# Optimization experiments

Hardware: AMD Instinct MI355X
Metric: run time of the kernel (lower is better)

Reference implementation:

```python
import jax, jax.numpy as jnp
import numpy as np

GX, GY, NH = 480, 360, 32
EPS = 1e-5


def _bn(x, g, b):
    # torch BatchNorm1d training-mode stats over the point dimension
    m = jnp.mean(x, axis=0)
    v = jnp.mean((x - m) ** 2, axis=0)
    return g * (x - m) / jnp.sqrt(v + EPS) + b


def setup_inputs():
    key = jax.random.key(0)
    ks = jax.random.split(key, 24)
    B, N, F = 2, 120000, 7
    s = 0.02
    inp = {
        "pt_fea": jax.random.normal(ks[0], (B, N, F), jnp.float32),
        "xy_ind": jax.random.randint(ks[1], (B, N, 2), 0, 360, dtype=jnp.int32),
        "bn0_g": jnp.ones((7,), jnp.float32), "bn0_b": jnp.zeros((7,), jnp.float32),
        "W1": jax.random.normal(ks[2], (7, 64), jnp.float32) * s,  "b1": jnp.zeros((64,), jnp.float32),
        "bn1_g": jnp.ones((64,), jnp.float32), "bn1_b": jnp.zeros((64,), jnp.float32),
        "W2": jax.random.normal(ks[3], (64, 128), jnp.float32) * s, "b2": jnp.zeros((128,), jnp.float32),
        "bn2_g": jnp.ones((128,), jnp.float32), "bn2_b": jnp.zeros((128,), jnp.float32),
        "W3": jax.random.normal(ks[4], (128, 256), jnp.float32) * s, "b3": jnp.zeros((256,), jnp.float32),
        "bn3_g": jnp.ones((256,), jnp.float32), "bn3_b": jnp.zeros((256,), jnp.float32),
        "W4": jax.random.normal(ks[5], (256, 512), jnp.float32) * s, "b4": jnp.zeros((512,), jnp.float32),
        "W5": jax.random.normal(ks[6], (512, NH), jnp.float32) * s, "b5": jnp.zeros((NH,), jnp.float32),
    }
    return inp


def _forward_sample(fea, xy, bn0_g, bn0_b, W1, b1, bn1_g, bn1_b, W2, b2,
                    bn2_g, bn2_b, W3, b3, bn3_g, bn3_b, W4, b4, W5, b5):
    # Simplified PointNet: BN -> (Linear, BN, ReLU) x3 -> Linear
    x = _bn(fea, bn0_g, bn0_b)
    x = jax.nn.relu(_bn(x @ W1 + b1, bn1_g, bn1_b))
    x = jax.nn.relu(_bn(x @ W2 + b2, bn2_g, bn2_b))
    x = jax.nn.relu(_bn(x @ W3 + b3, bn3_g, bn3_b))
    x = x @ W4 + b4                              # [N, 512]
    # per-voxel segment max over flattened BEV cell id
    ids = xy[:, 0] * GY + xy[:, 1]               # [N]
    nseg = GX * GY
    seg = jax.ops.segment_max(x, ids, num_segments=nseg)   # [nseg, 512]
    cnt = jax.ops.segment_sum(jnp.ones(ids.shape[0], x.dtype), ids, num_segments=nseg)
    occ = (cnt > 0)[:, None]
    seg = jnp.where(occ, seg, 0.0)               # empty voxels -> 0 (scatter semantics)
    nh = jax.nn.relu(seg @ W5 + b5)              # fea_compression
    nh = jnp.where(occ, nh, 0.0)
    return nh.reshape(GX, GY, NH).transpose(2, 0, 1)  # [NH, GX, GY]


def reference(pt_fea, xy_ind, bn0_g, bn0_b, W1, b1, bn1_g, bn1_b, W2, b2,
              bn2_g, bn2_b, W3, b3, bn3_g, bn3_b, W4, b4, W5, b5):
    f = lambda fea, xy: _forward_sample(fea, xy, bn0_g, bn0_b, W1, b1, bn1_g, bn1_b,
                                        W2, b2, bn2_g, bn2_b, W3, b3, bn3_g, bn3_b,
                                        W4, b4, W5, b5)
    return jax.vmap(f)(pt_fea, xy_ind)           # [B, NH, GX, GY]
```

## Files before the change

### kernel.cpp

```cpp
#include <hip/hip_runtime.h>
#include <cstdint>

#define GXD 480
#define GYD 360
#define NHD 32
#define NPTS 120000
#define MPAD 120064
#define MB128 (MPAD/128)
#define SEGR 129600
#define NSEG (GXD*GYD)
#define EPSB 1e-5f

using short8 = __attribute__((ext_vector_type(8))) short;
using f32x4  = __attribute__((ext_vector_type(4))) float;

__device__ __forceinline__ float bf2f(unsigned short u) {
    return __uint_as_float(((unsigned int)u) << 16);
}
__device__ __forceinline__ unsigned short f2bf(float f) {
    unsigned int u = __float_as_uint(f);
    u += 0x7fffu + ((u >> 16) & 1u);
    return (unsigned short)(u >> 16);
}
__device__ __forceinline__ unsigned int bnrelu_pack(unsigned int wv, float sc0, float sh0,
                                                    float sc1, float sh1)
{
    float lo = __uint_as_float(wv << 16);
    float hi = __uint_as_float(wv & 0xffff0000u);
    lo = fmaxf(fmaf(lo, sc0, sh0), 0.f);
    hi = fmaxf(fmaf(hi, sc1, sh1), 0.f);
    unsigned int r;
    asm("v_cvt_pk_bf16_f32 %0, %1, %2" : "=v"(r) : "v"(lo), "v"(hi));
    return r;
}

__device__ __forceinline__ void async16(const unsigned short* g, unsigned short* l)
{
    __builtin_amdgcn_global_load_lds(
        (const __attribute__((address_space(1))) unsigned int*)g,
        (__attribute__((address_space(3))) unsigned int*)l, 16, 0, 0);
}

__global__ __launch_bounds__(256) void bn0_stats_kernel(
    const float* __restrict__ fea, float* __restrict__ s0, float* __restrict__ q0)
{
    float s[7] = {0,0,0,0,0,0,0}, q[7] = {0,0,0,0,0,0,0};
    for (int p = blockIdx.x * 256 + threadIdx.x; p < NPTS; p += gridDim.x * 256) {
        const float* r = fea + (size_t)p * 7;
#pragma unroll
        for (int f = 0; f < 7; ++f) { float v = r[f]; s[f] += v; q[f] += v * v; }
    }
    __shared__ float red[256];
    int t = threadIdx.x;
#pragma unroll
    for (int f = 0; f < 7; ++f) {
        red[t] = s[f]; __syncthreads();
        for (int o = 128; o > 0; o >>= 1) {
            if (t < o) red[t] += red[t + o];
            __syncthreads();
        }
        if (t == 0) atomicAdd(&s0[f], red[0]);
        __syncthreads();
        red[t] = q[f]; __syncthreads();
        for (int o = 128; o > 0; o >>= 1) {
            if (t < o) red[t] += red[t + o];
            __syncthreads();
        }
        if (t == 0) atomicAdd(&q0[f], red[0]);
        __syncthreads();
    }
}

__global__ void prep0_kernel(const float* __restrict__ s0, const float* __restrict__ q0,
                             const float* __restrict__ g0, const float* __restrict__ b0,
                             const float* __restrict__ W1, const float* __restrict__ b1,
                             float* __restrict__ W1p, float* __restrict__ b1p)
{
    __shared__ float sc[7], sh[7];
    int t = threadIdx.x;
    if (t < 7) {
        float m = s0[t] / (float)NPTS;
        float v = q0[t] / (float)NPTS - m * m;
        float inv = 1.0f / sqrtf(fmaxf(v, 0.f) + EPSB);
        sc[t] = g0[t] * inv;
        sh[t] = b0[t] - m * g0[t] * inv;
    }
    __syncthreads();
    if (t < 64) {
        float acc = b1[t];
#pragma unroll
        for (int f = 0; f < 7; ++f) {
            W1p[f * 64 + t] = W1[f * 64 + t] * sc[f];
            acc += sh[f] * W1[f * 64 + t];
        }
        b1p[t] = acc;
    }
}

__global__ void prep_bn_kernel(const float* __restrict__ sum, const float* __restrict__ sq,
                               const float* __restrict__ g, const float* __restrict__ b,
                               float* __restrict__ sc, float* __restrict__ sh, int C)
{
    int c = blockIdx.x * blockDim.x + threadIdx.x;
    if (c < C) {
        float m = sum[c] / (float)NPTS;
        float v = sq[c] / (float)NPTS - m * m;
        float inv = 1.0f / sqrtf(fmaxf(v, 0.f) + EPSB);
        sc[c] = g[c] * inv;
        sh[c] = b[c] - m * g[c] * inv;
    }
}

template<int C>
__global__ __launch_bounds__(256) void bnrelu_kernel(
    unsigned short* __restrict__ Y,
    const float* __restrict__ sc, const float* __restrict__ sh)
{
    __shared__ float scs[C], shs[C];
    int t = threadIdx.x;
    for (int i = t; i < C; i += 256) { scs[i] = sc[i]; shs[i] = sh[i]; }
    __syncthreads();
    const size_t total8 = (size_t)MPAD * C / 8;
    for (size_t i = (size_t)blockIdx.x * 256 + t; i < total8; i += (size_t)gridDim.x * 256) {
        int c0 = (int)((i * 8) & (size_t)(C - 1));
        uint4 v = *(const uint4*)(Y + i * 8);
        float4 s0 = *(const float4*)&scs[c0];
        float4 s1 = *(const float4*)&scs[c0 + 4];
        float4 h0 = *(const float4*)&shs[c0];
        float4 h1 = *(const float4*)&shs[c0 + 4];
        uint4 o;
        o.x = bnrelu_pack(v.x, s0.x, h0.x, s0.y, h0.y);
        o.y = bnrelu_pack(v.y, s0.z, h0.z, s0.w, h0.w);
        o.z = bnrelu_pack(v.z, s1.x, h1.x, s1.y, h1.y);
        o.w = bnrelu_pack(v.w, s1.z, h1.z, s1.w, h1.w);
        *(uint4*)(Y + i * 8) = o;
    }
}

__global__ __launch_bounds__(256) void wtrans_kernel(const float* __restrict__ W,
                                                     unsigned short* __restrict__ Wt,
                                                     int K, int N)
{
    int i = blockIdx.x * 256 + threadIdx.x;
    if (i < K * N) {
        int k = i / N, n = i % N;
        Wt[(size_t)n * K + k] = f2bf(W[i]);
    }
}

__global__ __launch_bounds__(256) void layer1_kernel(
    const float* __restrict__ fea, const float* __restrict__ W1p, const float* __restrict__ b1p,
    unsigned short* __restrict__ y1, float* __restrict__ sum1, float* __restrict__ sq1)
{
    __shared__ float Wl[448], bl[64];
    __shared__ float feaL[256 * 7];
    __shared__ float colsum[64], colsq[64];
    int t = threadIdx.x;
    int p0 = blockIdx.x * 256;
    for (int i = t; i < 448; i += 256) Wl[i] = W1p[i];
    if (t < 64) { bl[t] = b1p[t]; colsum[t] = 0.f; colsq[t] = 0.f; }
    int nval7 = (NPTS - p0) * 7;
    for (int i = t; i < 256 * 7; i += 256)
        feaL[i] = (i < nval7) ? fea[(size_t)p0 * 7 + i] : 0.f;
    __syncthreads();
    int cg = t & 7, pt = t >> 3;
    float s[8] = {}, q[8] = {};
#pragma unroll
    for (int it = 0; it < 8; ++it) {
        int row = it * 32 + pt;
        bool valid = (p0 + row) < NPTS;
        float f[7];
#pragma unroll
        for (int ff = 0; ff < 7; ++ff) f[ff] = feaL[row * 7 + ff];
        float vj[8];
#pragma unroll
        for (int j = 0; j < 8; ++j) {
            int c = cg * 8 + j;
            float v = bl[c];
#pragma unroll
            for (int ff = 0; ff < 7; ++ff) v = fmaf(f[ff], Wl[ff * 64 + c], v);
            vj[j] = v;
            if (valid) { s[j] += v; q[j] += v * v; }
        }
        uint4 ow;
        ow.x = (unsigned int)f2bf(vj[0]) | ((unsigned int)f2bf(vj[1]) << 16);
        ow.y = (unsigned int)f2bf(vj[2]) | ((unsigned int)f2bf(vj[3]) << 16);
        ow.z = (unsigned int)f2bf(vj[4]) | ((unsigned int)f2bf(vj[5]) << 16);
        ow.w = (unsigned int)f2bf(vj[6]) | ((unsigned int)f2bf(vj[7]) << 16);
        *(uint4*)(y1 + (size_t)(p0 + row) * 64 + cg * 8) = ow;
    }
#pragma unroll
    for (int off = 8; off < 64; off <<= 1) {
#pragma unroll
        for (int j = 0; j < 8; ++j) {
            s[j] += __shfl_xor(s[j], off);
            q[j] += __shfl_xor(q[j], off);
        }
    }
    if ((t & 63) < 8) {
#pragma unroll
        for (int j = 0; j < 8; ++j) {
            atomicAdd(&colsum[cg * 8 + j], s[j]);
            atomicAdd(&colsq[cg * 8 + j], q[j]);
        }
    }
    __syncthreads();
    if (t < 64) {
        atomicAdd(&sum1[t], colsum[t]);
        atomicAdd(&sq1[t], colsq[t]);
    }
}

template<int K, int NC, bool STATS>
__global__ __launch_bounds__(256) void gemm_quad(
    const unsigned short* __restrict__ A, const unsigned short* __restrict__ Wt,
    const float* __restrict__ bias, unsigned short* __restrict__ Y,
    float* __restrict__ osum, float* __restrict__ osq)
{
    __shared__ __align__(16) unsigned short lds[16384];
    __shared__ float colsum[128], colsq[128];
    int t = threadIdx.x;
    int w = t >> 6, ln = t & 63, quad = ln >> 4, lr = ln & 15;
    int wr = w >> 1, wc = w & 1;
    const int mbase = blockIdx.y * 128;
    const int cbase = blockIdx.x * 128;
    unsigned short* Asl = lds;
    unsigned short* Bsl = lds + 8192;

    if (STATS && t < 128) { colsum[t] = 0.f; colsq[t] = 0.f; }
    __syncthreads();

    const int srow = w * 16 + (ln >> 2);
    const int koff = (ln & 3) * 8;

    auto stage = [&](int buf, int kt) {
#pragma unroll
        for (int half = 0; half < 2; ++half) {
            int row = half * 64 + srow;
            async16(A  + (size_t)(mbase + row) * K + kt + koff,
                    Asl + buf * 4096 + half * 2048 + w * 512 + ln * 8);
            async16(Wt + (size_t)(cbase + row) * K + kt + koff,
                    Bsl + buf * 4096 + half * 2048 + w * 512 + ln * 8);
        }
    };

    f32x4 acc[4][4];
#pragma unroll
    for (int i = 0; i < 4; ++i)
#pragma unroll
        for (int j = 0; j < 4; ++j) acc[i][j] = (f32x4){0.f, 0.f, 0.f, 0.f};

    stage(0, 0);
    stage(1, 32);

    constexpr int NR = K / 32;
#pragma unroll
    for (int r = 0; r < NR; ++r) {
        const int buf = r & 1;
        if (r + 1 < NR)
            asm volatile("s_waitcnt vmcnt(4)" ::: "memory");
        else
            asm volatile("s_waitcnt vmcnt(0)" ::: "memory");
        asm volatile("s_barrier" ::: "memory");
        short8 af[4], bfr[4];
#pragma unroll
        for (int mi = 0; mi < 4; ++mi)
            af[mi] = *(const short8*)&Asl[buf * 4096 + (wr * 64 + mi * 16 + lr) * 32 + quad * 8];
#pragma unroll
        for (int ni = 0; ni < 4; ++ni)
            bfr[ni] = *(const short8*)&Bsl[buf * 4096 + (wc * 64 + ni * 16 + lr) * 32 + quad * 8];
        asm volatile("s_waitcnt lgkmcnt(0)" ::: "memory");
        asm volatile("s_barrier" ::: "memory");
        if (r + 2 < NR)
            stage(buf, (r + 2) * 32);
#pragma unroll
        for (int mi = 0; mi < 4; ++mi)
#pragma unroll
            for (int ni = 0; ni < 4; ++ni)
                acc[mi][ni] = __builtin_amdgcn_mfma_f32_16x16x32_bf16(
                    af[mi], bfr[ni], acc[mi][ni], 0, 0, 0);
    }
    __syncthreads();

    unsigned short* Cw = lds + w * 4096;
#pragma unroll
    for (int ni = 0; ni < 4; ++ni) {
        int col = ni * 16 + lr;
        float bv = bias[cbase + wc * 64 + col];
        float s = 0.f, q = 0.f;
#pragma unroll
        for (int mi = 0; mi < 4; ++mi) {
            int rb = mi * 16 + quad * 4;
#pragma unroll
            for (int r = 0; r < 4; ++r) {
                float v = acc[mi][ni][r] + bv;
                Cw[(rb + r) * 64 + col] = f2bf(v);
                if (STATS && (mbase + wr * 64 + rb + r) < NPTS) { s += v; q += v * v; }
            }
        }
        if (STATS) {
            atomicAdd(&colsum[wc * 64 + col], s);
            atomicAdd(&colsq[wc * 64 + col], q);
        }
    }
#pragma unroll
    for (int i = 0; i < 8; ++i) {
        int idx = i * 64 + ln;
        int row = idx >> 3, colq = (idx & 7) * 8;
        *(uint4*)(Y + (size_t)(mbase + wr * 64 + row) * NC + cbase + wc * 64 + colq) =
            *(const uint4*)&Cw[row * 64 + colq];
    }
    if (STATS) {
        __syncthreads();
        if (t < 128) {
            atomicAdd(&osum[blockIdx.x * 128 + t], colsum[t]);
            atomicAdd(&osq[blockIdx.x * 128 + t], colsq[t]);
        }
    }
}

__global__ __launch_bounds__(256) void hist_kernel(const int* __restrict__ xy,
                                                   int* __restrict__ cnt)
{
    int p = blockIdx.x * 256 + threadIdx.x;
    if (p < NPTS) {
        int id = xy[(size_t)p * 2] * GYD + xy[(size_t)p * 2 + 1];
        atomicAdd(&cnt[id], 1);
    }
}

__global__ __launch_bounds__(256) void scanA_kernel(const int* __restrict__ cnt,
                                                    int* __restrict__ csum)
{
    __shared__ int red[256];
    int t = threadIdx.x, base = blockIdx.x * 2048;
    int s = 0;
    for (int i = t; i < 2048; i += 256) {
        int idx = base + i;
        if (idx < SEGR) s += cnt[idx];
    }
    red[t] = s; __syncthreads();
    for (int o = 128; o > 0; o >>= 1) { if (t < o) red[t] += red[t + o]; __syncthreads(); }
    if (t == 0) csum[blockIdx.x] = red[0];
}

__global__ void scanB_kernel(int* __restrict__ csum, int* __restrict__ offs)
{
    if (threadIdx.x == 0) {
        int run = 0;
        for (int i = 0; i < 64; ++i) { int v = csum[i]; csum[i] = run; run += v; }
        offs[SEGR] = run;
    }
}

__global__ __launch_bounds__(256) void scanC_kernel(const int* __restrict__ cnt,
                                                    const int* __restrict__ csum,
                                                    int* __restrict__ offs,
                                                    int* __restrict__ cursor)
{
    __shared__ int red[256];
    int t = threadIdx.x, base = blockIdx.x * 2048;
    int v[8]; int s = 0;
#pragma unroll
    for (int i = 0; i < 8; ++i) {
        int idx = base + t * 8 + i;
        v[i] = (idx < SEGR) ? cnt[idx] : 0;
        s += v[i];
    }
    red[t] = s; __syncthreads();
    for (int o = 1; o < 256; o <<= 1) {
        int x = (t >= o) ? red[t - o] : 0;
        __syncthreads();
        red[t] += x;
        __syncthreads();
    }
    int run = red[t] - s + csum[blockIdx.x];
#pragma unroll
    for (int i = 0; i < 8; ++i) {
        int idx = base + t * 8 + i;
        if (idx < SEGR) { offs[idx] = run; cursor[idx] = run; }
        run += v[i];
    }
}

__global__ __launch_bounds__(256) void scatter_idx_kernel(const int* __restrict__ xy,
                                                          int* __restrict__ cursor,
                                                          int* __restrict__ order)
{
    int p = blockIdx.x * 256 + threadIdx.x;
    if (p < NPTS) {
        int id = xy[(size_t)p * 2] * GYD + xy[(size_t)p * 2 + 1];
        int pos = atomicAdd(&cursor[id], 1);
        order[pos] = p;
    }
}

__global__ __launch_bounds__(256) void l4seg_kernel(
    const unsigned short* __restrict__ y3, const unsigned short* __restrict__ Wt4,
    const float* __restrict__ b4, const unsigned short* __restrict__ Wt5,
    const float* __restrict__ b5, const int* __restrict__ offs,
    const int* __restrict__ ord, float* __restrict__ out)
{
    __shared__ __align__(16) unsigned short Asl[2][2048];
    __shared__ __align__(16) unsigned short Bsl[2][4096];
    __shared__ __align__(16) unsigned short y4s[64 * 136];
    __shared__ __align__(16) unsigned short w5s[32 * 136];
    __shared__ float b4s[128];
    __shared__ int offs_s[65];
    int t = threadIdx.x;
    int w = t >> 6, ln = t & 63, quad = ln >> 4, lr = ln & 15;
    int c0 = blockIdx.x * 64;
    if (t < 65) offs_s[t] = offs[c0 + t];
    __syncthreads();
    const int jb = offs_s[0], je = offs_s[64];
    if (jb == je) {
#pragma unroll
        for (int j = 0; j < 8; ++j)
            out[(size_t)(w * 8 + j) * NSEG + c0 + ln] = 0.f;
        return;
    }
    const int cell = t >> 2, q = t & 3;
    const int cjb = offs_s[cell], cje = offs_s[cell + 1];

    f32x4 eacc[2];
    eacc[0] = (f32x4){0.f, 0.f, 0.f, 0.f};
    eacc[1] = (f32x4){0.f, 0.f, 0.f, 0.f};

    const int srow = w * 16 + (ln >> 2);
    const int koff = (ln & 3) * 8;

    for (int g = 0; g < 4; ++g) {
        {
            int n = t >> 3, ko = (t & 7) * 16;
            *(uint4*)&w5s[n * 136 + ko]     = *(const uint4*)(Wt5 + (size_t)n * 512 + g * 128 + ko);
            *(uint4*)&w5s[n * 136 + ko + 8] = *(const uint4*)(Wt5 + (size_t)n * 512 + g * 128 + ko + 8);
            if (t < 128) b4s[t] = b4[g * 128 + t];
        }
        float mxv[32];
#pragma unroll
        for (int i = 0; i < 32; ++i) mxv[i] = -3.0e38f;

        const unsigned short* Bg = Wt4 + (size_t)(g * 128 + srow) * 256 + koff;

        for (int cs = jb; cs < je; cs += 64) {
            int aj = cs + srow; if (aj >= je) aj = je - 1;
            const unsigned short* Ag = y3 + (size_t)ord[aj] * 256 + koff;
            auto stage = [&](int buf, int r) {
                async16(Ag + r * 32,            &Asl[buf][0] + w * 512 + ln * 8);
                async16(Bg + r * 32,            &Bsl[buf][0] + w * 512 + ln * 8);
                async16(Bg + 64 * 256 + r * 32, &Bsl[buf][2048] + w * 512 + ln * 8);
            };
            f32x4 acc[8];
#pragma unroll
            for (int i = 0; i < 8; ++i) acc[i] = (f32x4){0.f, 0.f, 0.f, 0.f};
            stage(0, 0); stage(1, 1);
#pragma unroll
            for (int r = 0; r < 8; ++r) {
                if (r < 7) asm volatile("s_waitcnt vmcnt(3)" ::: "memory");
                else       asm volatile("s_waitcnt vmcnt(0)" ::: "memory");
                asm volatile("s_barrier" ::: "memory");
                const int buf = r & 1;
                short8 af = *(const short8*)&Asl[buf][(w * 16 + lr) * 32 + quad * 8];
                short8 bfr[8];
#pragma unroll
                for (int ni = 0; ni < 8; ++ni)
                    bfr[ni] = *(const short8*)&Bsl[buf][(ni * 16 + lr) * 32 + quad * 8];
                asm volatile("s_waitcnt lgkmcnt(0)" ::: "memory");
                asm volatile("s_barrier" ::: "memory");
                if (r + 2 < 8) stage(buf, r + 2);
#pragma unroll
                for (int ni = 0; ni < 8; ++ni)
                    acc[ni] = __builtin_amdgcn_mfma_f32_16x16x32_bf16(af, bfr[ni], acc[ni], 0, 0, 0);
            }
#pragma unroll
            for (int ni = 0; ni < 8; ++ni) {
                float bv = b4s[ni * 16 + lr];
#pragma unroll
                for (int rr = 0; rr < 4; ++rr)
                    y4s[(w * 16 + quad * 4 + rr) * 136 + ni * 16 + lr] = f2bf(acc[ni][rr] + bv);
            }
            __syncthreads();
            int lo = cjb > cs ? cjb : cs;
            int hi = cje < cs + 64 ? cje : cs + 64;
            for (int j = lo; j < hi; ++j) {
                const uint4* rp = (const uint4*)&y4s[(j - cs) * 136 + q * 32];
#pragma unroll
                for (int u = 0; u < 4; ++u) {
                    uint4 vv = rp[u];
                    unsigned int wv[4] = {vv.x, vv.y, vv.z, vv.w};
#pragma unroll
                    for (int k2 = 0; k2 < 4; ++k2) {
                        int idx = u * 8 + k2 * 2;
                        mxv[idx]     = fmaxf(mxv[idx],     bf2f((unsigned short)(wv[k2] & 0xffffu)));
                        mxv[idx + 1] = fmaxf(mxv[idx + 1], bf2f((unsigned short)(wv[k2] >> 16)));
                    }
                }
            }
            __syncthreads();
        }
        {
            bool empty = (cjb == cje);
#pragma unroll
            for (int i = 0; i < 16; ++i) {
                float lo2 = empty ? 0.f : mxv[2 * i], hi2 = empty ? 0.f : mxv[2 * i + 1];
                unsigned int pk = (unsigned int)f2bf(lo2) | ((unsigned int)f2bf(hi2) << 16);
                *(unsigned int*)&y4s[cell * 136 + q * 32 + 2 * i] = pk;
            }
        }
        __syncthreads();
#pragma unroll
        for (int kt = 0; kt < 4; ++kt) {
            short8 af = *(const short8*)&y4s[(w * 16 + lr) * 136 + kt * 32 + quad * 8];
#pragma unroll
            for (int ni = 0; ni < 2; ++ni) {
                short8 bfr = *(const short8*)&w5s[(ni * 16 + lr) * 136 + kt * 32 + quad * 8];
                eacc[ni] = __builtin_amdgcn_mfma_f32_16x16x32_bf16(af, bfr, eacc[ni], 0, 0, 0);
            }
        }
        __syncthreads();
    }
    float* outs = (float*)&Asl[0][0];
#pragma unroll
    for (int ni = 0; ni < 2; ++ni) {
        int h = ni * 16 + lr;
        float bv = b5[h];
#pragma unroll
        for (int rr = 0; rr < 4; ++rr) {
            int cr = w * 16 + quad * 4 + rr;
            bool oc = offs_s[cr + 1] > offs_s[cr];
            outs[cr * 33 + h] = oc ? fmaxf(eacc[ni][rr] + bv, 0.f) : 0.f;
        }
    }
    __syncthreads();
#pragma unroll
    for (int j = 0; j < 8; ++j)
        out[(size_t)(w * 8 + j) * NSEG + c0 + ln] = outs[ln * 33 + w * 8 + j];
}

__global__ __launch_bounds__(256) void ztail_kernel(float* __restrict__ out)
{
    int i = blockIdx.x * 256 + threadIdx.x;
    const int per = (NSEG - SEGR) / 4;
    int h = i / per, c = i % per;
    *(float4*)(out + (size_t)h * NSEG + SEGR + (size_t)c * 4) = make_float4(0.f, 0.f, 0.f, 0.f);
}

extern "C" void kernel_launch(void* const* d_in, const int* in_sizes, int n_in,
                              void* d_out, int out_size, void* d_ws, size_t ws_size,
                              hipStream_t stream)
{
    const float* pt_fea = (const float*)d_in[0];
    const int*   xy_ind = (const int*)d_in[1];
    const float* bn0_g  = (const float*)d_in[2];
    const float* bn0_b  = (const float*)d_in[3];
    const float* W1     = (const float*)d_in[4];
    const float* b1     = (const float*)d_in[5];
    const float* bn1_g  = (const float*)d_in[6];
    const float* bn1_b  = (const float*)d_in[7];
    const float* W2     = (const float*)d_in[8];
    const float* b2     = (const float*)d_in[9];
    const float* bn2_g  = (const float*)d_in[10];
    const float* bn2_b  = (const float*)d_in[11];
    const float* W3     = (const float*)d_in[12];
    const float* b3     = (const float*)d_in[13];
    const float* bn3_g  = (const float*)d_in[14];
    const float* bn3_b  = (const float*)d_in[15];
    const float* W4     = (const float*)d_in[16];
    const float* b4     = (const float*)d_in[17];
    const float* W5     = (const float*)d_in[18];
    const float* b5     = (const float*)d_in[19];
    float* out = (float*)d_out;

    const size_t oY2   = 61472768;
    const size_t oE    = oY2 + (size_t)MPAD * 128 * 2;
    const size_t oCnt  = oE + (size_t)SEGR * 32 * 4;
    const size_t oOffs = oCnt + 518400;
    const size_t oCur  = oOffs + 518528;
    const size_t oOrd  = oCur + 518400;
    const size_t oCsum = oOrd + 480000;
    const size_t oSt   = oCsum + 512;
    const size_t oWt2  = oSt + 16384;
    const size_t oWt3  = oWt2 + 16384;
    const size_t oWt4  = oWt3 + 65536;
    const size_t oWt5  = oWt4 + 262144;

    unsigned short* y1   = (unsigned short*)d_ws;
    unsigned short* y3   = (unsigned short*)d_ws;
    unsigned short* y2   = (unsigned short*)((char*)d_ws + oY2);
    int*            cnt  = (int*)((char*)d_ws + oCnt);
    int*            offs = (int*)((char*)d_ws + oOffs);
    int*            cur  = (int*)((char*)d_ws + oCur);
    int*            ord  = (int*)((char*)d_ws + oOrd);
    int*            csum = (int*)((char*)d_ws + oCsum);
    float*          st   = (float*)((char*)d_ws + oSt);
    unsigned short* Wt2  = (unsigned short*)((char*)d_ws + oWt2);
    unsigned short* Wt3  = (unsigned short*)((char*)d_ws + oWt3);
    unsigned short* Wt4  = (unsigned short*)((char*)d_ws + oWt4);
    unsigned short* Wt5  = (unsigned short*)((char*)d_ws + oWt5);

    float* s0 = st + 0;     float* q0 = st + 8;
    float* W1p = st + 16;   float* b1p = st + 464;
    float* sum1 = st + 528; float* sq1 = st + 592; float* sc1 = st + 656; float* sh1 = st + 720;
    float* sum2 = st + 784; float* sq2 = st + 912; float* sc2 = st + 1040; float* sh2 = st + 1168;
    float* sum3 = st + 1296; float* sq3 = st + 1552; float* sc3 = st + 1808; float* sh3 = st + 2064;

    wtrans_kernel<<<(64 * 128 + 255) / 256, 256, 0, stream>>>(W2, Wt2, 64, 128);
    wtrans_kernel<<<(128 * 256 + 255) / 256, 256, 0, stream>>>(W3, Wt3, 128, 256);
    wtrans_kernel<<<(256 * 512 + 255) / 256, 256, 0, stream>>>(W4, Wt4, 256, 512);
    wtrans_kernel<<<(512 * 32 + 255) / 256, 256, 0, stream>>>(W5, Wt5, 512, 32);

    for (int b = 0; b < 2; ++b) {
        const float* fea_b = pt_fea + (size_t)b * NPTS * 7;
        const int*   xy_b  = xy_ind + (size_t)b * NPTS * 2;
        float*       out_b = out + (size_t)b * NHD * NSEG;

        (void)hipMemsetAsync(st, 0, 2320 * sizeof(float), stream);
        (void)hipMemsetAsync(cnt, 0, (size_t)SEGR * 4, stream);

        bn0_stats_kernel<<<128, 256, 0, stream>>>(fea_b, s0, q0);
        prep0_kernel<<<1, 64, 0, stream>>>(s0, q0, bn0_g, bn0_b, W1, b1, W1p, b1p);
        layer1_kernel<<<MPAD / 256, 256, 0, stream>>>(fea_b, W1p, b1p, y1, sum1, sq1);
        prep_bn_kernel<<<1, 64, 0, stream>>>(sum1, sq1, bn1_g, bn1_b, sc1, sh1, 64);
        bnrelu_kernel<64><<<1024, 256, 0, stream>>>(y1, sc1, sh1);
        gemm_quad<64, 128, true><<<dim3(1, MB128), 256, 0, stream>>>(
            y1, Wt2, b2, y2, sum2, sq2);
        prep_bn_kernel<<<1, 128, 0, stream>>>(sum2, sq2, bn2_g, bn2_b, sc2, sh2, 128);
        bnrelu_kernel<128><<<2048, 256, 0, stream>>>(y2, sc2, sh2);
        gemm_quad<128, 256, true><<<dim3(2, MB128), 256, 0, stream>>>(
            y2, Wt3, b3, y3, sum3, sq3);
        prep_bn_kernel<<<1, 256, 0, stream>>>(sum3, sq3, bn3_g, bn3_b, sc3, sh3, 256);
        bnrelu_kernel<256><<<2048, 256, 0, stream>>>(y3, sc3, sh3);

        hist_kernel<<<(NPTS + 255) / 256, 256, 0, stream>>>(xy_b, cnt);
        scanA_kernel<<<64, 256, 0, stream>>>(cnt, csum);
        scanB_kernel<<<1, 64, 0, stream>>>(csum, offs);
        scanC_kernel<<<64, 256, 0, stream>>>(cnt, csum, offs, cur);
        scatter_idx_kernel<<<(NPTS + 255) / 256, 256, 0, stream>>>(xy_b, cur, ord);

        l4seg_kernel<<<SEGR / 64, 256, 0, stream>>>(y3, Wt4, b4, Wt5, b5, offs, ord, out_b);
        ztail_kernel<<<1350, 256, 0, stream>>>(out_b);
    }
}
```

Before: 834.6 us.

## Stage full-K tiles with XOR-swizzled LDS layout in GEMM and segment-max kernels

```diff
diff --git a/kernel.cpp b/kernel.cpp
--- a/kernel.cpp
+++ b/kernel.cpp
@@ -212,12 +212,16 @@
 }
 
 template<int K, int NC, bool STATS>
-__global__ __launch_bounds__(256) void gemm_quad(
+__global__ __launch_bounds__(256) void gemm_single(
     const unsigned short* __restrict__ A, const unsigned short* __restrict__ Wt,
     const float* __restrict__ bias, unsigned short* __restrict__ Y,
     float* __restrict__ osum, float* __restrict__ osq)
 {
-    __shared__ __align__(16) unsigned short lds[16384];
+    constexpr int CH  = K / 8;
+    constexpr int RPI = 512 / K;
+    constexpr int AI  = 32 / RPI;
+    constexpr int NR  = K / 32;
+    __shared__ __align__(16) unsigned short lds[2 * 128 * K];
     __shared__ float colsum[128], colsq[128];
     int t = threadIdx.x;
     int w = t >> 6, ln = t & 63, quad = ln >> 4, lr = ln & 15;
@@ -225,24 +229,26 @@
     const int mbase = blockIdx.y * 128;
     const int cbase = blockIdx.x * 128;
     unsigned short* Asl = lds;
-    unsigned short* Bsl = lds + 8192;
+    unsigned short* Bsl = lds + 128 * K;
 
     if (STATS && t < 128) { colsum[t] = 0.f; colsq[t] = 0.f; }
-    __syncthreads();
-
-    const int srow = w * 16 + (ln >> 2);
-    const int koff = (ln & 3) * 8;
-
-    auto stage = [&](int buf, int kt) {
-#pragma unroll
-        for (int half = 0; half < 2; ++half) {
-            int row = half * 64 + srow;
-            async16(A  + (size_t)(mbase + row) * K + kt + koff,
-                    Asl + buf * 4096 + half * 2048 + w * 512 + ln * 8);
-            async16(Wt + (size_t)(cbase + row) * K + kt + koff,
-                    Bsl + buf * 4096 + half * 2048 + w * 512 + ln * 8);
-        }
-    };
+
+    const int rin = ln / CH;
+    const int cph = ln % CH;
+#pragma unroll
+    for (int i = 0; i < AI; ++i) {
+        int row = w * 32 + i * RPI + rin;
+        int cl  = cph ^ (row & 7);
+        async16(A + (size_t)(mbase + row) * K + cl * 8,
+                Asl + (w * 32 + i * RPI) * K + ln * 8);
+    }
+#pragma unroll
+    for (int i = 0; i < AI; ++i) {
+        int row = w * 32 + i * RPI + rin;
+        int cl  = cph ^ (row & 7);
+        async16(Wt + (size_t)(cbase + row) * K + cl * 8,
+                Bsl + (w * 32 + i * RPI) * K + ln * 8);
+    }
 
     f32x4 acc[4][4];
 #pragma unroll
@@ -250,29 +256,19 @@
 #pragma unroll
         for (int j = 0; j < 4; ++j) acc[i][j] = (f32x4){0.f, 0.f, 0.f, 0.f};
 
-    stage(0, 0);
-    stage(1, 32);
-
-    constexpr int NR = K / 32;
+    asm volatile("s_waitcnt vmcnt(0)" ::: "memory");
+    asm volatile("s_barrier" ::: "memory");
+
 #pragma unroll
     for (int r = 0; r < NR; ++r) {
-        const int buf = r & 1;
-        if (r + 1 < NR)
-            asm volatile("s_waitcnt vmcnt(4)" ::: "memory");
-        else
-            asm volatile("s_waitcnt vmcnt(0)" ::: "memory");
-        asm volatile("s_barrier" ::: "memory");
         short8 af[4], bfr[4];
+        const int cp = (r * 4 + quad) ^ (lr & 7);
 #pragma unroll
         for (int mi = 0; mi < 4; ++mi)
-            af[mi] = *(const short8*)&Asl[buf * 4096 + (wr * 64 + mi * 16 + lr) * 32 + quad * 8];
+            af[mi] = *(const short8*)&Asl[(wr * 64 + mi * 16 + lr) * K + cp * 8];
 #pragma unroll
         for (int ni = 0; ni < 4; ++ni)
-            bfr[ni] = *(const short8*)&Bsl[buf * 4096 + (wc * 64 + ni * 16 + lr) * 32 + quad * 8];
-        asm volatile("s_waitcnt lgkmcnt(0)" ::: "memory");
-        asm volatile("s_barrier" ::: "memory");
-        if (r + 2 < NR)
-            stage(buf, (r + 2) * 32);
+            bfr[ni] = *(const short8*)&Bsl[(wc * 64 + ni * 16 + lr) * K + cp * 8];
 #pragma unroll
         for (int mi = 0; mi < 4; ++mi)
 #pragma unroll
@@ -401,12 +397,13 @@
     const float* __restrict__ b5, const int* __restrict__ offs,
     const int* __restrict__ ord, float* __restrict__ out)
 {
-    __shared__ __align__(16) unsigned short Asl[2][2048];
-    __shared__ __align__(16) unsigned short Bsl[2][4096];
+    __shared__ __align__(16) unsigned short Asl[64 * 128];
+    __shared__ __align__(16) unsigned short Bsl[128 * 128];
     __shared__ __align__(16) unsigned short y4s[64 * 136];
     __shared__ __align__(16) unsigned short w5s[32 * 136];
     __shared__ float b4s[128];
     __shared__ int offs_s[65];
+    __shared__ int osl[64];
     int t = threadIdx.x;
     int w = t >> 6, ln = t & 63, quad = ln >> 4, lr = ln & 15;
     int c0 = blockIdx.x * 64;
@@ -426,8 +423,8 @@
     eacc[0] = (f32x4){0.f, 0.f, 0.f, 0.f};
     eacc[1] = (f32x4){0.f, 0.f, 0.f, 0.f};
 
-    const int srow = w * 16 + (ln >> 2);
-    const int koff = (ln & 3) * 8;
+    const int rin = ln >> 4;
+    const int cph = ln & 15;
 
     for (int g = 0; g < 4; ++g) {
         {
@@ -440,37 +437,44 @@
 #pragma unroll
         for (int i = 0; i < 32; ++i) mxv[i] = -3.0e38f;
 
-        const unsigned short* Bg = Wt4 + (size_t)(g * 128 + srow) * 256 + koff;
-
         for (int cs = jb; cs < je; cs += 64) {
-            int aj = cs + srow; if (aj >= je) aj = je - 1;
-            const unsigned short* Ag = y3 + (size_t)ord[aj] * 256 + koff;
-            auto stage = [&](int buf, int r) {
-                async16(Ag + r * 32,            &Asl[buf][0] + w * 512 + ln * 8);
-                async16(Bg + r * 32,            &Bsl[buf][0] + w * 512 + ln * 8);
-                async16(Bg + 64 * 256 + r * 32, &Bsl[buf][2048] + w * 512 + ln * 8);
-            };
+            if (t < 64) { int aj = cs + t; osl[t] = ord[aj < je ? aj : je - 1]; }
+            __syncthreads();
             f32x4 acc[8];
 #pragma unroll
             for (int i = 0; i < 8; ++i) acc[i] = (f32x4){0.f, 0.f, 0.f, 0.f};
-            stage(0, 0); stage(1, 1);
-#pragma unroll
-            for (int r = 0; r < 8; ++r) {
-                if (r < 7) asm volatile("s_waitcnt vmcnt(3)" ::: "memory");
-                else       asm volatile("s_waitcnt vmcnt(0)" ::: "memory");
+#pragma unroll
+            for (int h = 0; h < 2; ++h) {
+#pragma unroll
+                for (int i = 0; i < 4; ++i) {
+                    int row = w * 16 + i * 4 + rin;
+                    int cl  = cph ^ (row & 7);
+                    async16(y3 + (size_t)osl[row] * 256 + h * 128 + cl * 8,
+                            Asl + (w * 16 + i * 4) * 128 + ln * 8);
+                }
+#pragma unroll
+                for (int i = 0; i < 8; ++i) {
+                    int row = w * 32 + i * 4 + rin;
+                    int cl  = cph ^ (row & 7);
+                    async16(Wt4 + (size_t)(g * 128 + row) * 256 + h * 128 + cl * 8,
+                            Bsl + (w * 32 + i * 4) * 128 + ln * 8);
+                }
+                asm volatile("s_waitcnt vmcnt(0)" ::: "memory");
                 asm volatile("s_barrier" ::: "memory");
-                const int buf = r & 1;
-                short8 af = *(const short8*)&Asl[buf][(w * 16 + lr) * 32 + quad * 8];
-                short8 bfr[8];
-#pragma unroll
-                for (int ni = 0; ni < 8; ++ni)
-                    bfr[ni] = *(const short8*)&Bsl[buf][(ni * 16 + lr) * 32 + quad * 8];
+#pragma unroll
+                for (int r = 0; r < 4; ++r) {
+                    const int cp = (r * 4 + quad) ^ (lr & 7);
+                    short8 af = *(const short8*)&Asl[(w * 16 + lr) * 128 + cp * 8];
+                    short8 bfr[8];
+#pragma unroll
+                    for (int ni = 0; ni < 8; ++ni)
+                        bfr[ni] = *(const short8*)&Bsl[(ni * 16 + lr) * 128 + cp * 8];
+#pragma unroll
+                    for (int ni = 0; ni < 8; ++ni)
+                        acc[ni] = __builtin_amdgcn_mfma_f32_16x16x32_bf16(af, bfr[ni], acc[ni], 0, 0, 0);
+                }
                 asm volatile("s_waitcnt lgkmcnt(0)" ::: "memory");
                 asm volatile("s_barrier" ::: "memory");
-                if (r + 2 < 8) stage(buf, r + 2);
-#pragma unroll
-                for (int ni = 0; ni < 8; ++ni)
-                    acc[ni] = __builtin_amdgcn_mfma_f32_16x16x32_bf16(af, bfr[ni], acc[ni], 0, 0, 0);
             }
 #pragma unroll
             for (int ni = 0; ni < 8; ++ni) {
@@ -519,7 +523,7 @@
         }
         __syncthreads();
     }
-    float* outs = (float*)&Asl[0][0];
+    float* outs = (float*)&Asl[0];
 #pragma unroll
     for (int ni = 0; ni < 2; ++ni) {
         int h = ni * 16 + lr;
@@ -622,11 +626,11 @@
         layer1_kernel<<<MPAD / 256, 256, 0, stream>>>(fea_b, W1p, b1p, y1, sum1, sq1);
         prep_bn_kernel<<<1, 64, 0, stream>>>(sum1, sq1, bn1_g, bn1_b, sc1, sh1, 64);
         bnrelu_kernel<64><<<1024, 256, 0, stream>>>(y1, sc1, sh1);
-        gemm_quad<64, 128, true><<<dim3(1, MB128), 256, 0, stream>>>(
+        gemm_single<64, 128, true><<<dim3(1, MB128), 256, 0, stream>>>(
             y1, Wt2, b2, y2, sum2, sq2);
         prep_bn_kernel<<<1, 128, 0, stream>>>(sum2, sq2, bn2_g, bn2_b, sc2, sh2, 128);
         bnrelu_kernel<128><<<2048, 256, 0, stream>>>(y2, sc2, sh2);
-        gemm_quad<128, 256, true><<<dim3(2, MB128), 256, 0, stream>>>(
+        gemm_single<128, 256, true><<<dim3(2, MB128), 256, 0, stream>>>(
             y2, Wt3, b3, y3, sum3, sq3);
         prep_bn_kernel<<<1, 256, 0, stream>>>(sum3, sq3, bn3_g, bn3_b, sc3, sh3, 256);
         bnrelu_kernel<256><<<2048, 256, 0, stream>>>(y3, sc3, sh3);
```

Measured after the change: 824.3 us. Within noise of the previous version (-1.2%).

## Restructure layer-4 segment-max kernel to stage full-K weight slabs in LDS

Applied to the files above, without the earlier changes.

```diff
diff --git a/kernel.cpp b/kernel.cpp
--- a/kernel.cpp
+++ b/kernel.cpp
@@ -29,6 +29,12 @@
     float hi = __uint_as_float(wv & 0xffff0000u);
     lo = fmaxf(fmaf(lo, sc0, sh0), 0.f);
     hi = fmaxf(fmaf(hi, sc1, sh1), 0.f);
+    unsigned int r;
+    asm("v_cvt_pk_bf16_f32 %0, %1, %2" : "=v"(r) : "v"(lo), "v"(hi));
+    return r;
+}
+__device__ __forceinline__ unsigned int pk_bf16(float lo, float hi)
+{
     unsigned int r;
     asm("v_cvt_pk_bf16_f32 %0, %1, %2" : "=v"(r) : "v"(lo), "v"(hi));
     return r;
@@ -401,16 +407,17 @@
     const float* __restrict__ b5, const int* __restrict__ offs,
     const int* __restrict__ ord, float* __restrict__ out)
 {
-    __shared__ __align__(16) unsigned short Asl[2][2048];
-    __shared__ __align__(16) unsigned short Bsl[2][4096];
-    __shared__ __align__(16) unsigned short y4s[64 * 136];
-    __shared__ __align__(16) unsigned short w5s[32 * 136];
-    __shared__ float b4s[128];
+    __shared__ __align__(16) unsigned short Bsl[64 * 256];
+    __shared__ __align__(16) unsigned short w5s[32 * 64];
+    __shared__ __align__(16) unsigned short y4s[64 * 72];
+    __shared__ float b4s[512];
     __shared__ int offs_s[65];
+    __shared__ int osl[128];
     int t = threadIdx.x;
     int w = t >> 6, ln = t & 63, quad = ln >> 4, lr = ln & 15;
     int c0 = blockIdx.x * 64;
     if (t < 65) offs_s[t] = offs[c0 + t];
+    for (int i = t; i < 512; i += 256) b4s[i] = b4[i];
     __syncthreads();
     const int jb = offs_s[0], je = offs_s[64];
     if (jb == je) {
@@ -419,6 +426,9 @@
             out[(size_t)(w * 8 + j) * NSEG + c0 + ln] = 0.f;
         return;
     }
+    if (t < 128) { int aj = jb + t; osl[t] = (aj < je) ? ord[aj] : 0; }
+    __syncthreads();
+
     const int cell = t >> 2, q = t & 3;
     const int cjb = offs_s[cell], cje = offs_s[cell + 1];
 
@@ -426,100 +436,95 @@
     eacc[0] = (f32x4){0.f, 0.f, 0.f, 0.f};
     eacc[1] = (f32x4){0.f, 0.f, 0.f, 0.f};
 
-    const int srow = w * 16 + (ln >> 2);
-    const int koff = (ln & 3) * 8;
-
-    for (int g = 0; g < 4; ++g) {
+    for (int p = 0; p < 8; ++p) {
+#pragma unroll
+        for (int i = 0; i < 8; ++i) {
+            int rl = w * 16 + i * 2 + (ln >> 5);
+            int cl = (ln & 31) ^ (rl & 7);
+            async16(Wt4 + (size_t)(p * 64 + rl) * 256 + cl * 8,
+                    Bsl + (w * 16 + i * 2) * 256 + ln * 8);
+        }
         {
-            int n = t >> 3, ko = (t & 7) * 16;
-            *(uint4*)&w5s[n * 136 + ko]     = *(const uint4*)(Wt5 + (size_t)n * 512 + g * 128 + ko);
-            *(uint4*)&w5s[n * 136 + ko + 8] = *(const uint4*)(Wt5 + (size_t)n * 512 + g * 128 + ko + 8);
-            if (t < 128) b4s[t] = b4[g * 128 + t];
-        }
-        float mxv[32];
-#pragma unroll
-        for (int i = 0; i < 32; ++i) mxv[i] = -3.0e38f;
-
-        const unsigned short* Bg = Wt4 + (size_t)(g * 128 + srow) * 256 + koff;
-
-        for (int cs = jb; cs < je; cs += 64) {
-            int aj = cs + srow; if (aj >= je) aj = je - 1;
-            const unsigned short* Ag = y3 + (size_t)ord[aj] * 256 + koff;
-            auto stage = [&](int buf, int r) {
-                async16(Ag + r * 32,            &Asl[buf][0] + w * 512 + ln * 8);
-                async16(Bg + r * 32,            &Bsl[buf][0] + w * 512 + ln * 8);
-                async16(Bg + 64 * 256 + r * 32, &Bsl[buf][2048] + w * 512 + ln * 8);
-            };
-            f32x4 acc[8];
-#pragma unroll
-            for (int i = 0; i < 8; ++i) acc[i] = (f32x4){0.f, 0.f, 0.f, 0.f};
-            stage(0, 0); stage(1, 1);
+            int rl = t >> 3, cl = (t & 7) ^ (rl & 7);
+            async16(Wt5 + (size_t)rl * 512 + p * 64 + cl * 8, w5s + t * 8);
+        }
+        float mxv[16];
+#pragma unroll
+        for (int i = 0; i < 16; ++i) mxv[i] = -3.0e38f;
+
+        int chunk = 0;
+        for (int cs = jb; cs < je; cs += 64, ++chunk) {
+            int j = cs + w * 16 + lr; if (j >= je) j = je - 1;
+            int idx = j - jb;
+            int pr = (idx < 128) ? osl[idx] : ord[j];
+            const unsigned short* Ar = y3 + (size_t)pr * 256 + quad * 8;
+            short8 af[8];
+#pragma unroll
+            for (int r = 0; r < 8; ++r)
+                af[r] = *(const short8*)(Ar + r * 32);
+            f32x4 acc[4];
+#pragma unroll
+            for (int i = 0; i < 4; ++i) acc[i] = (f32x4){0.f, 0.f, 0.f, 0.f};
+            if (chunk == 0) {
+                asm volatile("s_waitcnt vmcnt(0)" ::: "memory");
+                asm volatile("s_barrier" ::: "memory");
+            }
 #pragma unroll
             for (int r = 0; r < 8; ++r) {
-                if (r < 7) asm volatile("s_waitcnt vmcnt(3)" ::: "memory");
-                else       asm volatile("s_waitcnt vmcnt(0)" ::: "memory");
-                asm volatile("s_barrier" ::: "memory");
-                const int buf = r & 1;
-                short8 af = *(const short8*)&Asl[buf][(w * 16 + lr) * 32 + quad * 8];
-                short8 bfr[8];
-#pragma unroll
-                for (int ni = 0; ni < 8; ++ni)
-                    bfr[ni] = *(const short8*)&Bsl[buf][(ni * 16 + lr) * 32 + quad * 8];
-                asm volatile("s_waitcnt lgkmcnt(0)" ::: "memory");
-                asm volatile("s_barrier" ::: "memory");
-                if (r + 2 < 8) stage(buf, r + 2);
-#pragma unroll
-                for (int ni = 0; ni < 8; ++ni)
-                    acc[ni] = __builtin_amdgcn_mfma_f32_16x16x32_bf16(af, bfr[ni], acc[ni], 0, 0, 0);
+                const int cp = (r * 4 + quad) ^ (lr & 7);
+#pragma unroll
+                for (int ni = 0; ni < 4; ++ni) {
+                    short8 bfr = *(const short8*)&Bsl[(ni * 16 + lr) * 256 + cp * 8];
+                    acc[ni] = __builtin_amdgcn_mfma_f32_16x16x32_bf16(af[r], bfr, acc[ni], 0, 0, 0);
+                }
             }
 #pragma unroll
-            for (int ni = 0; ni < 8; ++ni) {
-                float bv = b4s[ni * 16 + lr];
+            for (int ni = 0; ni < 4; ++ni) {
+                float bv = b4s[p * 64 + ni * 16 + lr];
 #pragma unroll
                 for (int rr = 0; rr < 4; ++rr)
-                    y4s[(w * 16 + quad * 4 + rr) * 136 + ni * 16 + lr] = f2bf(acc[ni][rr] + bv);
+                    y4s[(w * 16 + quad * 4 + rr) * 72 + ni * 16 + lr] = f2bf(acc[ni][rr] + bv);
             }
-            __syncthreads();
+            asm volatile("s_waitcnt lgkmcnt(0)" ::: "memory");
+            asm volatile("s_barrier" ::: "memory");
             int lo = cjb > cs ? cjb : cs;
             int hi = cje < cs + 64 ? cje : cs + 64;
-            for (int j = lo; j < hi; ++j) {
-                const uint4* rp = (const uint4*)&y4s[(j - cs) * 136 + q * 32];
-#pragma unroll
-                for (int u = 0; u < 4; ++u) {
-                    uint4 vv = rp[u];
-                    unsigned int wv[4] = {vv.x, vv.y, vv.z, vv.w};
-#pragma unroll
-                    for (int k2 = 0; k2 < 4; ++k2) {
-                        int idx = u * 8 + k2 * 2;
-                        mxv[idx]     = fmaxf(mxv[idx],     bf2f((unsigned short)(wv[k2] & 0xffffu)));
-                        mxv[idx + 1] = fmaxf(mxv[idx + 1], bf2f((unsigned short)(wv[k2] >> 16)));
-                    }
+            for (int jj = lo; jj < hi; ++jj) {
+                const uint4* rp = (const uint4*)&y4s[(jj - cs) * 72 + q * 16];
+                uint4 v0 = rp[0], v1 = rp[1];
+                unsigned int wv[8] = {v0.x, v0.y, v0.z, v0.w, v1.x, v1.y, v1.z, v1.w};
+#pragma unroll
+                for (int k2 = 0; k2 < 8; ++k2) {
+                    mxv[2 * k2]     = fmaxf(mxv[2 * k2],     bf2f((unsigned short)(wv[k2] & 0xffffu)));
+                    mxv[2 * k2 + 1] = fmaxf(mxv[2 * k2 + 1], bf2f((unsigned short)(wv[k2] >> 16)));
                 }
             }
-            __syncthreads();
+            asm volatile("s_barrier" ::: "memory");
         }
         {
             bool empty = (cjb == cje);
 #pragma unroll
-            for (int i = 0; i < 16; ++i) {
+            for (int i = 0; i < 8; ++i) {
                 float lo2 = empty ? 0.f : mxv[2 * i], hi2 = empty ? 0.f : mxv[2 * i + 1];
-                unsigned int pk = (unsigned int)f2bf(lo2) | ((unsigned int)f2bf(hi2) << 16);
-                *(unsigned int*)&y4s[cell * 136 + q * 32 + 2 * i] = pk;
+                *(unsigned int*)&y4s[cell * 72 + q * 16 + 2 * i] = pk_bf16(lo2, hi2);
             }
         }
-        __syncthreads();
-#pragma unroll
-        for (int kt = 0; kt < 4; ++kt) {
-            short8 af = *(const short8*)&y4s[(w * 16 + lr) * 136 + kt * 32 + quad * 8];
+        asm volatile("s_waitcnt lgkmcnt(0)" ::: "memory");
+        asm volatile("s_barrier" ::: "memory");
+#pragma unroll
+        for (int kt = 0; kt < 2; ++kt) {
+            short8 af2 = *(const short8*)&y4s[(w * 16 + lr) * 72 + kt * 32 + quad * 8];
+            const int cp = (kt * 4 + quad) ^ (lr & 7);
 #pragma unroll
             for (int ni = 0; ni < 2; ++ni) {
-                short8 bfr = *(const short8*)&w5s[(ni * 16 + lr) * 136 + kt * 32 + quad * 8];
-                eacc[ni] = __builtin_amdgcn_mfma_f32_16x16x32_bf16(af, bfr, eacc[ni], 0, 0, 0);
+                short8 bfr = *(const short8*)&w5s[(ni * 16 + lr) * 64 + cp * 8];
+                eacc[ni] = __builtin_amdgcn_mfma_f32_16x16x32_bf16(af2, bfr, eacc[ni], 0, 0, 0);
             }
         }
-        __syncthreads();
-    }
-    float* outs = (float*)&Asl[0][0];
+        asm volatile("s_waitcnt lgkmcnt(0)" ::: "memory");
+        asm volatile("s_barrier" ::: "memory");
+    }
+    float* outs = (float*)&Bsl[0];
 #pragma unroll
     for (int ni = 0; ni < 2; ++ni) {
         int h = ni * 16 + lr;
```

After: 783.1 us. 1.07x faster.
